# Performance work log

Measured on AMD Instinct MI355X. Metric: run time of the kernel, lower is better.

Reference implementation:

```python
import jax, jax.numpy as jnp
import numpy as np

B, C, H, W = 8, 256, 64, 64
NUM_HEADS = 8
HEAD_DIM = C // NUM_HEADS  # 32
KSIZE = 3
DILATIONS = [1, 2, 3, 4]
SCALE = HEAD_DIM ** -0.5


def _unfold(x, k, dil):
    # x: (B, d, H, W) -> (B, d, k*k, H, W), matching torch nn.Unfold with
    # padding = dil*(k-1)//2 and channel-major patch ordering.
    p = dil * (k - 1) // 2
    xp = jnp.pad(x, ((0, 0), (0, 0), (p, p), (p, p)))
    h, w = x.shape[2], x.shape[3]
    patches = [xp[:, :, i * dil:i * dil + h, j * dil:j * dil + w]
               for i in range(k) for j in range(k)]
    return jnp.stack(patches, axis=2)


def setup_inputs() -> dict:
    key = jax.random.key(0)
    k1, k2, k3, k4, k5 = jax.random.split(key, 5)
    x = jax.random.normal(k1, (B, C, H, W), dtype=jnp.float32)
    w_qkv = jax.random.normal(k2, (3 * C, C), dtype=jnp.float32) * 0.02
    b_qkv = jnp.zeros((3 * C,), dtype=jnp.float32)
    w_proj = jax.random.normal(k3, (C, C), dtype=jnp.float32) * 0.02
    b_proj = jnp.zeros((C,), dtype=jnp.float32)
    return {"x": x, "w_qkv": w_qkv, "b_qkv": b_qkv,
            "w_proj": w_proj, "b_proj": b_proj}


def reference(x, w_qkv, b_qkv, w_proj, b_proj):
    b, c, h, w = x.shape
    # 1x1 conv qkv projection
    qkv = jnp.einsum('bchw,oc->bohw', x, w_qkv) + b_qkv[None, :, None, None]
    qkv = qkv.reshape(b, 3, NUM_HEADS, HEAD_DIM, h, w)
    outs = []
    for hd in range(NUM_HEADS):  # small fixed loop; heads structurally distinct (dilation)
        dil = DILATIONS[hd % len(DILATIONS)]
        q = qkv[:, 0, hd]   # (B, d, H, W)
        k_ = qkv[:, 1, hd]
        v = qkv[:, 2, hd]
        kk = _unfold(k_, KSIZE, dil)  # (B, d, K2, H, W)
        vv = _unfold(v, KSIZE, dil)
        attn = jax.nn.softmax(
            jnp.einsum('bdhw,bdKhw->bKhw', q, kk) * SCALE, axis=1)
        outs.append(jnp.einsum('bKhw,bdKhw->bdhw', attn, vv))
    # torch.stack(dim=1).reshape(B,C,H,W) => head-major channel concat
    out = jnp.concatenate(outs, axis=1)  # (B, C, H, W)
    out = jnp.einsum('bchw,oc->bohw', out, w_proj) + b_proj[None, :, None, None]
    return out
```

## Files before the change

kernel.cpp:

```cpp
#include <hip/hip_runtime.h>
#include <cstdint>

typedef unsigned short ushortT;
typedef __attribute__((ext_vector_type(8))) short short8;
typedef __attribute__((ext_vector_type(8))) unsigned short ushort8v;
typedef __attribute__((ext_vector_type(4))) float float4v;

#define ATT_SCALE 0.17677669529663687f

__device__ inline float bf2f(unsigned short u) {
    union { unsigned int i; float f; } x; x.i = ((unsigned int)u) << 16; return x.f;
}
__device__ inline unsigned short f2bf(float f) {
    union { float f; unsigned int i; } x; x.f = f;
    unsigned int i = x.i;
    i += 0x7fffu + ((i >> 16) & 1u);
    return (unsigned short)(i >> 16);
}

__device__ inline void gld_lds16(const ushortT* g, ushortT* l) {
    __builtin_amdgcn_global_load_lds((const __attribute__((address_space(1))) void*)g,
                                     (__attribute__((address_space(3))) void*)l, 16, 0, 0);
}

__global__ __launch_bounds__(256) void transpose_cp(const float* __restrict__ x,
                                                    ushortT* __restrict__ xT,
                                                    const float* __restrict__ w_qkv,
                                                    const float* __restrict__ w_proj,
                                                    const float* __restrict__ b_qkv,
                                                    const float* __restrict__ b_proj,
                                                    ushortT* __restrict__ wqkvB,
                                                    ushortT* __restrict__ wprojB,
                                                    float* __restrict__ bqF,
                                                    float* __restrict__ bpF) {
    __shared__ __align__(16) ushortT tile[64][65];
    const int b  = blockIdx.z;
    const int c0 = blockIdx.x * 64;
    const int p0 = blockIdx.y * 64;
    const int t  = threadIdx.x;

    {
        int flat = blockIdx.x + 4 * blockIdx.y + 256 * blockIdx.z;
        if (flat < 1028) {
            int i = flat * 256 + t;
            if (i < 196608) {
                wqkvB[i] = f2bf(w_qkv[i]);
            } else if (i < 262144) {
                wprojB[i - 196608] = f2bf(w_proj[i - 196608]);
            } else if (i < 262912) {
                bqF[i - 262144] = b_qkv[i - 262144];
            } else if (i < 263168) {
                bpF[i - 262912] = b_proj[i - 262912];
            }
        }
    }

    const float* xb = x + (size_t)b * 256 * 4096;
#pragma unroll
    for (int it = 0; it < 4; it++) {
        int id  = t + it * 256;
        int row = id >> 4;
        int c4  = (id & 15) * 4;
        float4 v = *(const float4*)(xb + (size_t)(c0 + row) * 4096 + p0 + c4);
        tile[row][c4 + 0] = f2bf(v.x);
        tile[row][c4 + 1] = f2bf(v.y);
        tile[row][c4 + 2] = f2bf(v.z);
        tile[row][c4 + 3] = f2bf(v.w);
    }
    __syncthreads();
    ushortT* xTb = xT + (size_t)b * 4096 * 256;
#pragma unroll
    for (int it = 0; it < 2; it++) {
        int id   = t + it * 256;
        int prow = id >> 3;
        int cc   = (id & 7) * 8;
        ushort8v v;
#pragma unroll
        for (int j = 0; j < 8; j++) v[j] = tile[cc + j][prow];
        *(ushort8v*)(xTb + (size_t)(p0 + prow) * 256 + c0 + cc) = v;
    }
}

__global__ __launch_bounds__(256) void gemm_bt(const ushortT* __restrict__ A,
                                               const ushortT* __restrict__ Bt, long long sBb,
                                               int ldb, int bHeadMajor,
                                               void* __restrict__ D, long long sDb,
                                               int ldd, int dHeadMajor, int outF32,
                                               const float* __restrict__ bias, int biasAlongM,
                                               int K, int swizzleMode) {
    __shared__ __align__(16) ushortT pool[16384];

    int mIdx, nIdx, bz;
    {
        int id = blockIdx.x;
        int r  = id & 7;
        int j  = id >> 3;
        if (swizzleMode == 0) {
            mIdx = r * 32 + j / 6;
            nIdx = j % 6;
            bz   = 0;
        } else {
            int p = r * 32 + (j >> 1);
            bz   = p >> 5;
            nIdx = p & 31;
            mIdx = j & 1;
        }
    }
    const int n0 = nIdx * 128;
    const int m0 = mIdx * 128;
    Bt += (size_t)bz * sBb;

    const int t    = threadIdx.x;
    const int wv   = t >> 6;
    const int lane = t & 63;
    const int lm   = lane & 15;
    const int quad = lane >> 4;
    const int wm   = wv & 1;
    const int wn   = wv >> 1;

    ushortT* Als = pool;
    ushortT* Bls = pool + 8192;

    float4v acc[4][4];
#pragma unroll
    for (int i = 0; i < 4; i++)
#pragma unroll
        for (int j = 0; j < 4; j++) { float4v z = {0.f, 0.f, 0.f, 0.f}; acc[i][j] = z; }

    const int nkt = K >> 6;
    for (int kt = 0; kt < nkt; ++kt) {
        __syncthreads();
#pragma unroll
        for (int j = 0; j < 4; j++) {
            int cid = wv * 256 + j * 64 + lane;
            int row = cid >> 3;
            int s   = cid & 7;
            int gc  = s ^ (row & 7);
            const ushortT* ga = A + (size_t)(m0 + row) * K + kt * 64 + gc * 8;
            const ushortT* gb = bHeadMajor
                ? Bt + ((size_t)(kt * 2 + (gc >> 2)) * 32768 + (n0 + row)) * 32 + (gc & 3) * 8
                : Bt + (size_t)(n0 + row) * ldb + kt * 64 + gc * 8;
            gld_lds16(ga, Als + (size_t)(wv * 256 + j * 64) * 8);
            gld_lds16(gb, Bls + (size_t)(wv * 256 + j * 64) * 8);
        }
        asm volatile("s_waitcnt vmcnt(0)" ::: "memory");
        __syncthreads();

#pragma unroll
        for (int g = 0; g < 2; g++) {
            short8 af[4], bfr[4];
#pragma unroll
            for (int i = 0; i < 4; i++) {
                int r = wm * 64 + i * 16 + lm;
                int slot = (g * 4 + quad) ^ (r & 7);
                af[i] = *(const short8*)&Als[r * 64 + slot * 8];
            }
#pragma unroll
            for (int j = 0; j < 4; j++) {
                int r = wn * 64 + j * 16 + lm;
                int slot = (g * 4 + quad) ^ (r & 7);
                bfr[j] = *(const short8*)&Bls[r * 64 + slot * 8];
            }
#pragma unroll
            for (int i = 0; i < 4; i++)
#pragma unroll
                for (int j = 0; j < 4; j++)
                    acc[i][j] = __builtin_amdgcn_mfma_f32_16x16x32_bf16(af[i], bfr[j], acc[i][j], 0, 0, 0);
        }
    }

    if (dHeadMajor) {
        __syncthreads();
#pragma unroll
        for (int i = 0; i < 4; i++) {
#pragma unroll
            for (int j = 0; j < 4; j++) {
                int c = wn * 64 + j * 16 + lm;
#pragma unroll
                for (int rg = 0; rg < 4; rg++) {
                    int r = wm * 64 + i * 16 + quad * 4 + rg;
                    float v = acc[i][j][rg] + bias[biasAlongM ? (m0 + r) : (n0 + c)];
                    int chunk = (c >> 3) ^ (r & 7);
                    pool[r * 128 + chunk * 8 + (c & 7)] = f2bf(v);
                }
            }
        }
        __syncthreads();
        ushortT* Dh = (ushortT*)D + (size_t)bz * sDb;
#pragma unroll
        for (int g = 0; g < 4; g++) {
            ushortT* base = Dh + ((size_t)((n0 >> 5) + g) * 32768 + m0) * 32;
#pragma unroll
            for (int it = 0; it < 2; it++) {
                int id = it * 256 + t;
                int r  = id >> 2;
                int cb = id & 3;
                int pch = (g * 4 + cb) ^ (r & 7);
                ushort8v v = *(const ushort8v*)&pool[r * 128 + pch * 8];
                *(ushort8v*)(base + r * 32 + cb * 8) = v;
            }
        }
    } else if (outF32) {
        float* poolF = (float*)pool;
        float* Df = (float*)D + (size_t)bz * sDb;
#pragma unroll
        for (int pass = 0; pass < 2; pass++) {
            __syncthreads();
            if (wm == pass) {
#pragma unroll
                for (int i = 0; i < 4; i++) {
#pragma unroll
                    for (int j = 0; j < 4; j++) {
                        int c = wn * 64 + j * 16 + lm;
#pragma unroll
                        for (int rg = 0; rg < 4; rg++) {
                            int r64 = i * 16 + quad * 4 + rg;
                            float v = acc[i][j][rg] +
                                      bias[biasAlongM ? (m0 + pass * 64 + r64) : (n0 + c)];
                            int phys = (c + 4 * r64) & 127;
                            poolF[r64 * 128 + phys] = v;
                        }
                    }
                }
            }
            __syncthreads();
#pragma unroll
            for (int it = 0; it < 8; it++) {
                int id  = it * 256 + t;
                int r64 = id >> 5;
                int c   = (id & 31) * 4;
                int phys = (c + 4 * r64) & 127;
                float4 v = *(const float4*)&poolF[r64 * 128 + phys];
                *(float4*)&Df[(size_t)(m0 + pass * 64 + r64) * ldd + n0 + c] = v;
            }
        }
    } else {
        ushortT* Dh = (ushortT*)D + (size_t)bz * sDb;
#pragma unroll
        for (int i = 0; i < 4; i++) {
            int r0 = m0 + wm * 64 + i * 16 + quad * 4;
#pragma unroll
            for (int j = 0; j < 4; j++) {
                int c = n0 + wn * 64 + j * 16 + lm;
#pragma unroll
                for (int rg = 0; rg < 4; rg++) {
                    int r = r0 + rg;
                    float v = acc[i][j][rg] + bias[biasAlongM ? r : c];
                    Dh[(size_t)r * ldd + c] = f2bf(v);
                }
            }
        }
    }
}

__global__ __launch_bounds__(256, 8) void attn_k(ushortT* qkv) {
    const int gt      = blockIdx.x * 256 + threadIdx.x;
    const int quarter = gt & 3;
    const int pix     = gt >> 2;
    const int hd      = pix >> 15;
    const int rem     = pix & 32767;
    const int b       = rem >> 12;
    const int p       = rem & 4095;
    const int h       = p >> 6;
    const int w       = p & 63;
    const int dil     = (hd & 3) + 1;
    const int c0      = quarter * 8;

    ushortT*       qp    = qkv + ((size_t)hd * 32768 + (size_t)b * 4096 + p) * 32 + c0;
    const ushortT* kbase = qkv + ((size_t)(8  + hd) * 32768 + (size_t)b * 4096) * 32 + c0;
    const ushortT* vbase = qkv + ((size_t)(16 + hd) * 32768 + (size_t)b * 4096) * 32 + c0;

    float q[8];
    {
        ushort8v v = *(const ushort8v*)qp;
#pragma unroll
        for (int j = 0; j < 8; j++) q[j] = bf2f(v[j]);
    }

    float lgt[9];
    int   nb[9];
    unsigned vmask = 0;
#pragma unroll
    for (int ii = 0; ii < 3; ii++) {
#pragma unroll
        for (int jj = 0; jj < 3; jj++) {
            int idx = ii * 3 + jj;
            int hh = h + (ii - 1) * dil;
            int ww = w + (jj - 1) * dil;
            bool ok = ((unsigned)hh < 64u) && ((unsigned)ww < 64u);
            int pp = (hh << 6) + ww;
            nb[idx] = pp;
            float l = 0.f;
            if (ok) {
                vmask |= (1u << idx);
                ushort8v v = *(const ushort8v*)(kbase + (size_t)pp * 32);
#pragma unroll
                for (int j = 0; j < 8; j++) l += q[j] * bf2f(v[j]);
            }
            lgt[idx] = l;
        }
    }
#pragma unroll
    for (int i = 0; i < 9; i++) {
        float l = lgt[i];
        l += __shfl_xor(l, 1);
        l += __shfl_xor(l, 2);
        lgt[i] = l * ATT_SCALE;
    }

    float mx = lgt[0];
#pragma unroll
    for (int i = 1; i < 9; i++) mx = fmaxf(mx, lgt[i]);
    float e[9], s = 0.f;
#pragma unroll
    for (int i = 0; i < 9; i++) { e[i] = __expf(lgt[i] - mx); s += e[i]; }
    const float inv = 1.f / s;

    float acc[8];
#pragma unroll
    for (int d = 0; d < 8; d++) acc[d] = 0.f;
#pragma unroll
    for (int idx = 0; idx < 9; idx++) {
        if ((vmask >> idx) & 1u) {
            float pj = e[idx] * inv;
            ushort8v v = *(const ushort8v*)(vbase + (size_t)nb[idx] * 32);
#pragma unroll
            for (int j = 0; j < 8; j++) acc[j] += pj * bf2f(v[j]);
        }
    }

    {
        ushort8v v;
#pragma unroll
        for (int j = 0; j < 8; j++) v[j] = f2bf(acc[j]);
        *(ushort8v*)qp = v;
    }
}

extern "C" void kernel_launch(void* const* d_in, const int* in_sizes, int n_in,
                              void* d_out, int out_size, void* d_ws, size_t ws_size,
                              hipStream_t stream) {
    const float* x      = (const float*)d_in[0];
    const float* w_qkv  = (const float*)d_in[1];
    const float* b_qkv  = (const float*)d_in[2];
    const float* w_proj = (const float*)d_in[3];
    const float* b_proj = (const float*)d_in[4];

    char* ws = (char*)d_ws;
    float*   bqF    = (float*)(ws + 256);
    float*   bpF    = (float*)(ws + 3328);
    ushortT* wqkvB  = (ushortT*)(ws + 4352);
    ushortT* wprojB = (ushortT*)(ws + 397568);
    ushortT* qkv    = (ushortT*)(ws + 528640);
    ushortT* xT     = (ushortT*)d_out;

    transpose_cp<<<dim3(4, 64, 8), 256, 0, stream>>>(x, xT, w_qkv, w_proj, b_qkv, b_proj,
                                                     wqkvB, wprojB, bqF, bpF);

    gemm_bt<<<dim3(1536), 256, 0, stream>>>(xT, wqkvB, 0, 256, 0,
                                            qkv, 0, 0, 1, 0,
                                            bqF, 0, 256, 0);

    attn_k<<<dim3(4096), 256, 0, stream>>>(qkv);

    gemm_bt<<<dim3(512), 256, 0, stream>>>(wprojB, qkv, (long long)4096 * 32, 0, 1,
                                           d_out, (long long)256 * 4096, 4096, 0, 1,
                                           bpF, 1, 256, 1);
}
```

Measured before the change: 153.1 us.

## Fuse fp32-to-bf16 conversion and transpose into GEMM tile loads, drop prep kernel

Removes the separate transpose/convert kernel. The GEMMs now read fp32 x and fp32 weights directly, converting to bf16 with packed converts while staging into LDS, and the x tile is transposed on the fly. This eliminates one launch and a round trip of the bf16 xT and weight copies through global memory. The cost is that A/B loads now go through registers instead of async global-to-LDS loads, and the weights are reconverted by every block.

```diff
diff --git a/kernel.cpp b/kernel.cpp
--- a/kernel.cpp
+++ b/kernel.cpp
@@ -5,6 +5,7 @@
 typedef __attribute__((ext_vector_type(8))) short short8;
 typedef __attribute__((ext_vector_type(8))) unsigned short ushort8v;
 typedef __attribute__((ext_vector_type(4))) float float4v;
+typedef __attribute__((ext_vector_type(4))) unsigned int uint4v;
 
 #define ATT_SCALE 0.17677669529663687f
 
@@ -17,73 +18,21 @@
     i += 0x7fffu + ((i >> 16) & 1u);
     return (unsigned short)(i >> 16);
 }
+__device__ inline unsigned int cvtpk_bf16(float a, float b) {
+    unsigned int r;
+    asm("v_cvt_pk_bf16_f32 %0, %1, %2" : "=v"(r) : "v"(a), "v"(b));
+    return r;
+}
 
 __device__ inline void gld_lds16(const ushortT* g, ushortT* l) {
     __builtin_amdgcn_global_load_lds((const __attribute__((address_space(1))) void*)g,
                                      (__attribute__((address_space(3))) void*)l, 16, 0, 0);
 }
 
-__global__ __launch_bounds__(256) void transpose_cp(const float* __restrict__ x,
-                                                    ushortT* __restrict__ xT,
-                                                    const float* __restrict__ w_qkv,
-                                                    const float* __restrict__ w_proj,
-                                                    const float* __restrict__ b_qkv,
-                                                    const float* __restrict__ b_proj,
-                                                    ushortT* __restrict__ wqkvB,
-                                                    ushortT* __restrict__ wprojB,
-                                                    float* __restrict__ bqF,
-                                                    float* __restrict__ bpF) {
-    __shared__ __align__(16) ushortT tile[64][65];
-    const int b  = blockIdx.z;
-    const int c0 = blockIdx.x * 64;
-    const int p0 = blockIdx.y * 64;
-    const int t  = threadIdx.x;
-
-    {
-        int flat = blockIdx.x + 4 * blockIdx.y + 256 * blockIdx.z;
-        if (flat < 1028) {
-            int i = flat * 256 + t;
-            if (i < 196608) {
-                wqkvB[i] = f2bf(w_qkv[i]);
-            } else if (i < 262144) {
-                wprojB[i - 196608] = f2bf(w_proj[i - 196608]);
-            } else if (i < 262912) {
-                bqF[i - 262144] = b_qkv[i - 262144];
-            } else if (i < 263168) {
-                bpF[i - 262912] = b_proj[i - 262912];
-            }
-        }
-    }
-
-    const float* xb = x + (size_t)b * 256 * 4096;
-#pragma unroll
-    for (int it = 0; it < 4; it++) {
-        int id  = t + it * 256;
-        int row = id >> 4;
-        int c4  = (id & 15) * 4;
-        float4 v = *(const float4*)(xb + (size_t)(c0 + row) * 4096 + p0 + c4);
-        tile[row][c4 + 0] = f2bf(v.x);
-        tile[row][c4 + 1] = f2bf(v.y);
-        tile[row][c4 + 2] = f2bf(v.z);
-        tile[row][c4 + 3] = f2bf(v.w);
-    }
-    __syncthreads();
-    ushortT* xTb = xT + (size_t)b * 4096 * 256;
-#pragma unroll
-    for (int it = 0; it < 2; it++) {
-        int id   = t + it * 256;
-        int prow = id >> 3;
-        int cc   = (id & 7) * 8;
-        ushort8v v;
-#pragma unroll
-        for (int j = 0; j < 8; j++) v[j] = tile[cc + j][prow];
-        *(ushort8v*)(xTb + (size_t)(p0 + prow) * 256 + c0 + cc) = v;
-    }
-}
-
-__global__ __launch_bounds__(256) void gemm_bt(const ushortT* __restrict__ A,
-                                               const ushortT* __restrict__ Bt, long long sBb,
-                                               int ldb, int bHeadMajor,
+template<int AMODE, int BMODE>
+__global__ __launch_bounds__(256) void gemm_bt(const void* __restrict__ Av,
+                                               const void* __restrict__ Bv, long long sBb,
+                                               int ldb,
                                                void* __restrict__ D, long long sDb,
                                                int ldd, int dHeadMajor, int outF32,
                                                const float* __restrict__ bias, int biasAlongM,
@@ -108,7 +57,6 @@
     }
     const int n0 = nIdx * 128;
     const int m0 = mIdx * 128;
-    Bt += (size_t)bz * sBb;
 
     const int t    = threadIdx.x;
     const int wv   = t >> 6;
@@ -121,6 +69,23 @@
     ushortT* Als = pool;
     ushortT* Bls = pool + 8192;
 
+    const float*   Axf = nullptr;
+    int            pb  = 0;
+    const float*   Awf = nullptr;
+    const ushortT* Bh  = nullptr;
+    const float*   Bwf = nullptr;
+    if constexpr (AMODE == 2) {
+        Axf = (const float*)Av + (size_t)(m0 >> 12) * (256 * 4096);
+        pb  = m0 & 4095;
+    } else {
+        Awf = (const float*)Av;
+    }
+    if constexpr (BMODE == 1) {
+        Bh = (const ushortT*)Bv + (size_t)bz * sBb;
+    } else {
+        Bwf = (const float*)Bv;
+    }
+
     float4v acc[4][4];
 #pragma unroll
     for (int i = 0; i < 4; i++)
@@ -130,20 +95,75 @@
     const int nkt = K >> 6;
     for (int kt = 0; kt < nkt; ++kt) {
         __syncthreads();
-#pragma unroll
-        for (int j = 0; j < 4; j++) {
-            int cid = wv * 256 + j * 64 + lane;
-            int row = cid >> 3;
-            int s   = cid & 7;
-            int gc  = s ^ (row & 7);
-            const ushortT* ga = A + (size_t)(m0 + row) * K + kt * 64 + gc * 8;
-            const ushortT* gb = bHeadMajor
-                ? Bt + ((size_t)(kt * 2 + (gc >> 2)) * 32768 + (n0 + row)) * 32 + (gc & 3) * 8
-                : Bt + (size_t)(n0 + row) * ldb + kt * 64 + gc * 8;
-            gld_lds16(ga, Als + (size_t)(wv * 256 + j * 64) * 8);
-            gld_lds16(gb, Bls + (size_t)(wv * 256 + j * 64) * 8);
-        }
-        asm volatile("s_waitcnt vmcnt(0)" ::: "memory");
+
+        if constexpr (AMODE == 2) {
+            const int pg = t & 31;
+            const int cg = t >> 5;
+            const float* xs = Axf + (size_t)(kt * 64 + cg * 8) * 4096 + pb + pg * 4;
+            float4v ld[8];
+#pragma unroll
+            for (int i = 0; i < 8; i++) ld[i] = *(const float4v*)(xs + (size_t)i * 4096);
+#pragma unroll
+            for (int j = 0; j < 4; j++) {
+                int r = pg * 4 + j;
+                int s = cg ^ (r & 7);
+                uint4v w;
+                w.x = cvtpk_bf16(ld[0][j], ld[1][j]);
+                w.y = cvtpk_bf16(ld[2][j], ld[3][j]);
+                w.z = cvtpk_bf16(ld[4][j], ld[5][j]);
+                w.w = cvtpk_bf16(ld[6][j], ld[7][j]);
+                *(uint4v*)&Als[r * 64 + s * 8] = w;
+            }
+        } else if constexpr (AMODE == 1) {
+#pragma unroll
+            for (int j = 0; j < 4; j++) {
+                int u  = t + 256 * j;
+                int r  = u >> 3;
+                int gc = u & 7;
+                const float* gp = Awf + (size_t)(m0 + r) * K + kt * 64 + gc * 8;
+                float4v a = *(const float4v*)gp;
+                float4v b = *(const float4v*)(gp + 4);
+                uint4v w;
+                w.x = cvtpk_bf16(a[0], a[1]);
+                w.y = cvtpk_bf16(a[2], a[3]);
+                w.z = cvtpk_bf16(b[0], b[1]);
+                w.w = cvtpk_bf16(b[2], b[3]);
+                *(uint4v*)&Als[r * 64 + (gc ^ (r & 7)) * 8] = w;
+            }
+        }
+
+        if constexpr (BMODE == 1) {
+#pragma unroll
+            for (int j = 0; j < 4; j++) {
+                int cid = wv * 256 + j * 64 + lane;
+                int row = cid >> 3;
+                int s   = cid & 7;
+                int gc  = s ^ (row & 7);
+                const ushortT* gb =
+                    Bh + ((size_t)(kt * 2 + (gc >> 2)) * 32768 + (n0 + row)) * 32 + (gc & 3) * 8;
+                gld_lds16(gb, Bls + (size_t)(wv * 256 + j * 64) * 8);
+            }
+        } else if constexpr (BMODE == 2) {
+#pragma unroll
+            for (int j = 0; j < 4; j++) {
+                int u  = t + 256 * j;
+                int r  = u >> 3;
+                int gc = u & 7;
+                const float* gp = Bwf + (size_t)(n0 + r) * K + kt * 64 + gc * 8;
+                float4v a = *(const float4v*)gp;
+                float4v b = *(const float4v*)(gp + 4);
+                uint4v w;
+                w.x = cvtpk_bf16(a[0], a[1]);
+                w.y = cvtpk_bf16(a[2], a[3]);
+                w.z = cvtpk_bf16(b[0], b[1]);
+                w.w = cvtpk_bf16(b[2], b[3]);
+                *(uint4v*)&Bls[r * 64 + (gc ^ (r & 7)) * 8] = w;
+            }
+        }
+
+        if constexpr (BMODE == 1) {
+            asm volatile("s_waitcnt vmcnt(0)" ::: "memory");
+        }
         __syncthreads();
 
 #pragma unroll
@@ -230,8 +250,8 @@
                 int r64 = id >> 5;
                 int c   = (id & 31) * 4;
                 int phys = (c + 4 * r64) & 127;
-                float4 v = *(const float4*)&poolF[r64 * 128 + phys];
-                *(float4*)&Df[(size_t)(m0 + pass * 64 + r64) * ldd + n0 + c] = v;
+                float4v v = *(const float4v*)&poolF[r64 * 128 + phys];
+                *(float4v*)&Df[(size_t)(m0 + pass * 64 + r64) * ldd + n0 + c] = v;
             }
         }
     } else {
@@ -346,24 +366,15 @@
     const float* w_proj = (const float*)d_in[3];
     const float* b_proj = (const float*)d_in[4];
 
-    char* ws = (char*)d_ws;
-    float*   bqF    = (float*)(ws + 256);
-    float*   bpF    = (float*)(ws + 3328);
-    ushortT* wqkvB  = (ushortT*)(ws + 4352);
-    ushortT* wprojB = (ushortT*)(ws + 397568);
-    ushortT* qkv    = (ushortT*)(ws + 528640);
-    ushortT* xT     = (ushortT*)d_out;
-
-    transpose_cp<<<dim3(4, 64, 8), 256, 0, stream>>>(x, xT, w_qkv, w_proj, b_qkv, b_proj,
-                                                     wqkvB, wprojB, bqF, bpF);
-
-    gemm_bt<<<dim3(1536), 256, 0, stream>>>(xT, wqkvB, 0, 256, 0,
-                                            qkv, 0, 0, 1, 0,
-                                            bqF, 0, 256, 0);
+    ushortT* qkv = (ushortT*)d_ws;
+
+    gemm_bt<2, 2><<<dim3(1536), 256, 0, stream>>>(x, w_qkv, 0, 256,
+                                                  qkv, 0, 0, 1, 0,
+                                                  b_qkv, 0, 256, 0);
 
     attn_k<<<dim3(4096), 256, 0, stream>>>(qkv);
 
-    gemm_bt<<<dim3(512), 256, 0, stream>>>(wprojB, qkv, (long long)4096 * 32, 0, 1,
-                                           d_out, (long long)256 * 4096, 4096, 0, 1,
-                                           bpF, 1, 256, 1);
-}
+    gemm_bt<1, 1><<<dim3(512), 256, 0, stream>>>(w_proj, qkv, (long long)4096 * 32, 0,
+                                                 d_out, (long long)256 * 4096, 4096, 0, 1,
+                                                 b_proj, 1, 256, 1);
+}
```

New measurement: 160.2 us. +4.6%, slower.

## Double-buffer LDS staging in output projection GEMM and trim attention registers

Applied to the files above, without the earlier changes.

Templates the GEMM on a double-buffer flag and enables it for the output projection, so the next K tile's global-to-LDS loads are issued before the current tile's MFMAs and waited on with a partial vmcnt. This is meant to hide global load latency in the projection GEMM, where only 512 blocks run. It doubles LDS use to 64KB per block, which may lower occupancy. The attention kernel also recomputes neighbour indices and reuses the logits array for the exponentials to reduce register pressure.

```diff
diff --git a/kernel.cpp b/kernel.cpp
--- a/kernel.cpp
+++ b/kernel.cpp
@@ -81,6 +81,7 @@
     }
 }
 
+template<int DBUF>
 __global__ __launch_bounds__(256) void gemm_bt(const ushortT* __restrict__ A,
                                                const ushortT* __restrict__ Bt, long long sBb,
                                                int ldb, int bHeadMajor,
@@ -88,7 +89,7 @@
                                                int ldd, int dHeadMajor, int outF32,
                                                const float* __restrict__ bias, int biasAlongM,
                                                int K, int swizzleMode) {
-    __shared__ __align__(16) ushortT pool[16384];
+    __shared__ __align__(16) ushortT pool[DBUF ? 32768 : 16384];
 
     int mIdx, nIdx, bz;
     {
@@ -118,9 +119,6 @@
     const int wm   = wv & 1;
     const int wn   = wv >> 1;
 
-    ushortT* Als = pool;
-    ushortT* Bls = pool + 8192;
-
     float4v acc[4][4];
 #pragma unroll
     for (int i = 0; i < 4; i++)
@@ -128,8 +126,8 @@
         for (int j = 0; j < 4; j++) { float4v z = {0.f, 0.f, 0.f, 0.f}; acc[i][j] = z; }
 
     const int nkt = K >> 6;
-    for (int kt = 0; kt < nkt; ++kt) {
-        __syncthreads();
+
+    auto stageFn = [&](int kt, ushortT* Ad, ushortT* Bd) {
 #pragma unroll
         for (int j = 0; j < 4; j++) {
             int cid = wv * 256 + j * 64 + lane;
@@ -140,12 +138,11 @@
             const ushortT* gb = bHeadMajor
                 ? Bt + ((size_t)(kt * 2 + (gc >> 2)) * 32768 + (n0 + row)) * 32 + (gc & 3) * 8
                 : Bt + (size_t)(n0 + row) * ldb + kt * 64 + gc * 8;
-            gld_lds16(ga, Als + (size_t)(wv * 256 + j * 64) * 8);
-            gld_lds16(gb, Bls + (size_t)(wv * 256 + j * 64) * 8);
-        }
-        asm volatile("s_waitcnt vmcnt(0)" ::: "memory");
-        __syncthreads();
-
+            gld_lds16(ga, Ad + (size_t)(wv * 256 + j * 64) * 8);
+            gld_lds16(gb, Bd + (size_t)(wv * 256 + j * 64) * 8);
+        }
+    };
+    auto mmaFn = [&](const ushortT* Als, const ushortT* Bls) {
 #pragma unroll
         for (int g = 0; g < 2; g++) {
             short8 af[4], bfr[4];
@@ -166,6 +163,34 @@
 #pragma unroll
                 for (int j = 0; j < 4; j++)
                     acc[i][j] = __builtin_amdgcn_mfma_f32_16x16x32_bf16(af[i], bfr[j], acc[i][j], 0, 0, 0);
+        }
+    };
+
+    if constexpr (DBUF) {
+        stageFn(0, pool, pool + 8192);
+        for (int kt = 0; kt < nkt; ++kt) {
+            const int cur = kt & 1;
+            ushortT* Ac = pool + cur * 16384;
+            if (kt + 1 < nkt) {
+                ushortT* An = pool + (cur ^ 1) * 16384;
+                stageFn(kt + 1, An, An + 8192);
+                asm volatile("s_waitcnt vmcnt(8)" ::: "memory");
+            } else {
+                asm volatile("s_waitcnt vmcnt(0)" ::: "memory");
+            }
+            __builtin_amdgcn_s_barrier();
+            asm volatile("" ::: "memory");
+            mmaFn(Ac, Ac + 8192);
+            asm volatile("" ::: "memory");
+            __builtin_amdgcn_s_barrier();
+        }
+    } else {
+        for (int kt = 0; kt < nkt; ++kt) {
+            __syncthreads();
+            stageFn(kt, pool, pool + 8192);
+            asm volatile("s_waitcnt vmcnt(0)" ::: "memory");
+            __syncthreads();
+            mmaFn(pool, pool + 8192);
         }
     }
 
@@ -230,8 +255,8 @@
                 int r64 = id >> 5;
                 int c   = (id & 31) * 4;
                 int phys = (c + 4 * r64) & 127;
-                float4 v = *(const float4*)&poolF[r64 * 128 + phys];
-                *(float4*)&Df[(size_t)(m0 + pass * 64 + r64) * ldd + n0 + c] = v;
+                float4v v = *(const float4v*)&poolF[r64 * 128 + phys];
+                *(float4v*)&Df[(size_t)(m0 + pass * 64 + r64) * ldd + n0 + c] = v;
             }
         }
     } else {
@@ -278,27 +303,22 @@
     }
 
     float lgt[9];
-    int   nb[9];
     unsigned vmask = 0;
 #pragma unroll
-    for (int ii = 0; ii < 3; ii++) {
-#pragma unroll
-        for (int jj = 0; jj < 3; jj++) {
-            int idx = ii * 3 + jj;
-            int hh = h + (ii - 1) * dil;
-            int ww = w + (jj - 1) * dil;
-            bool ok = ((unsigned)hh < 64u) && ((unsigned)ww < 64u);
-            int pp = (hh << 6) + ww;
-            nb[idx] = pp;
-            float l = 0.f;
-            if (ok) {
-                vmask |= (1u << idx);
-                ushort8v v = *(const ushort8v*)(kbase + (size_t)pp * 32);
-#pragma unroll
-                for (int j = 0; j < 8; j++) l += q[j] * bf2f(v[j]);
-            }
-            lgt[idx] = l;
-        }
+    for (int idx = 0; idx < 9; idx++) {
+        const int ii = idx / 3 - 1;
+        const int jj = idx % 3 - 1;
+        int hh = h + ii * dil;
+        int ww = w + jj * dil;
+        bool ok = ((unsigned)hh < 64u) && ((unsigned)ww < 64u);
+        float l = 0.f;
+        if (ok) {
+            vmask |= (1u << idx);
+            ushort8v v = *(const ushort8v*)(kbase + (size_t)((hh << 6) + ww) * 32);
+#pragma unroll
+            for (int j = 0; j < 8; j++) l += q[j] * bf2f(v[j]);
+        }
+        lgt[idx] = l;
     }
 #pragma unroll
     for (int i = 0; i < 9; i++) {
@@ -311,9 +331,9 @@
     float mx = lgt[0];
 #pragma unroll
     for (int i = 1; i < 9; i++) mx = fmaxf(mx, lgt[i]);
-    float e[9], s = 0.f;
-#pragma unroll
-    for (int i = 0; i < 9; i++) { e[i] = __expf(lgt[i] - mx); s += e[i]; }
+    float s = 0.f;
+#pragma unroll
+    for (int i = 0; i < 9; i++) { lgt[i] = __expf(lgt[i] - mx); s += lgt[i]; }
     const float inv = 1.f / s;
 
     float acc[8];
@@ -322,8 +342,12 @@
 #pragma unroll
     for (int idx = 0; idx < 9; idx++) {
         if ((vmask >> idx) & 1u) {
-            float pj = e[idx] * inv;
-            ushort8v v = *(const ushort8v*)(vbase + (size_t)nb[idx] * 32);
+            const int ii = idx / 3 - 1;
+            const int jj = idx % 3 - 1;
+            int hh = h + ii * dil;
+            int ww = w + jj * dil;
+            float pj = lgt[idx] * inv;
+            ushort8v v = *(const ushort8v*)(vbase + (size_t)((hh << 6) + ww) * 32);
 #pragma unroll
             for (int j = 0; j < 8; j++) acc[j] += pj * bf2f(v[j]);
         }
@@ -357,13 +381,13 @@
     transpose_cp<<<dim3(4, 64, 8), 256, 0, stream>>>(x, xT, w_qkv, w_proj, b_qkv, b_proj,
                                                      wqkvB, wprojB, bqF, bpF);
 
-    gemm_bt<<<dim3(1536), 256, 0, stream>>>(xT, wqkvB, 0, 256, 0,
-                                            qkv, 0, 0, 1, 0,
-                                            bqF, 0, 256, 0);
+    gemm_bt<0><<<dim3(1536), 256, 0, stream>>>(xT, wqkvB, 0, 256, 0,
+                                               qkv, 0, 0, 1, 0,
+                                               bqF, 0, 256, 0);
 
     attn_k<<<dim3(4096), 256, 0, stream>>>(qkv);
 
-    gemm_bt<<<dim3(512), 256, 0, stream>>>(wprojB, qkv, (long long)4096 * 32, 0, 1,
-                                           d_out, (long long)256 * 4096, 4096, 0, 1,
-                                           bpF, 1, 256, 1);
-}
+    gemm_bt<1><<<dim3(512), 256, 0, stream>>>(wprojB, qkv, (long long)4096 * 32, 0, 1,
+                                              d_out, (long long)256 * 4096, 4096, 0, 1,
+                                              bpF, 1, 256, 1);
+}
```

After: 160.5 us. +4.8%, slower.
